# Kernel tuning notes

Hardware: AMD Instinct MI355X
Metric: run time of the kernel (lower is better)

The kernel has to match this reference:

```python
import jax, jax.numpy as jnp
import numpy as np

N_NODES = 50000
N_EDGES = 600000
N_GRAPHS = 64


def _linear_init(key, fan_in, fan_out):
    # torch nn.Linear default: U(-1/sqrt(fan_in), 1/sqrt(fan_in))
    s = 1.0 / np.sqrt(fan_in)
    kw, kb = jax.random.split(key)
    W = jax.random.uniform(kw, (fan_in, fan_out), jnp.float32, -s, s)
    b = jax.random.uniform(kb, (fan_out,), jnp.float32, -s, s)
    return W, b


def setup_inputs() -> dict:
    key = jax.random.key(0)
    ks = jax.random.split(key, 7)
    x = jax.random.normal(ks[0], (N_NODES, 128), jnp.float32)
    edge_index = jax.random.randint(ks[1], (2, N_EDGES), 0, N_NODES, dtype=jnp.int32).astype(jnp.int64)
    batch = jnp.sort(jax.random.randint(ks[2], (N_NODES,), 0, N_GRAPHS, dtype=jnp.int32)).astype(jnp.int64)
    W1, b1 = _linear_init(ks[3], 128, 256)
    W2, b2 = _linear_init(ks[4], 256, 256)
    W3, b3 = _linear_init(ks[5], 256, 128)
    W4, b4 = _linear_init(ks[6], 128, 10)
    return dict(x=x, edge_index=edge_index, batch=batch,
                W1=W1, b1=b1, W2=W2, b2=b2, W3=W3, b3=b3, W4=W4, b4=b4)


def _gcn_conv(h, src, dst, W, b, n_nodes):
    # PyG GCNConv: add self-loops (src/dst already include them),
    # symmetric normalization D^{-1/2} (A+I) D^{-1/2} h W + b.
    h = h @ W                                      # [N, Cout]
    deg = jax.ops.segment_sum(jnp.ones(src.shape[0], h.dtype), dst, num_segments=n_nodes)
    dinv = jnp.where(deg > 0, jax.lax.rsqrt(deg), 0.0)
    norm = dinv[src] * dinv[dst]                   # [E+N]
    msg = h[src] * norm[:, None]                   # gather + scale per edge
    agg = jax.ops.segment_sum(msg, dst, num_segments=n_nodes)  # scatter-add
    return agg + b


def reference(x, edge_index, batch, W1, b1, W2, b2, W3, b3, W4, b4):
    n = x.shape[0]
    loops = jnp.arange(n, dtype=edge_index.dtype)
    src = jnp.concatenate([edge_index[0], loops])
    dst = jnp.concatenate([edge_index[1], loops])
    # GCNBlock (activate_last=True since dense layers follow)
    h = jax.nn.relu(_gcn_conv(x, src, dst, W1, b1, n))
    h = jax.nn.relu(_gcn_conv(h, src, dst, W2, b2, n))
    # global_mean_pool over batch segments
    sums = jax.ops.segment_sum(h, batch, num_segments=N_GRAPHS)          # [G, 256]
    counts = jax.ops.segment_sum(jnp.ones((n,), h.dtype), batch, num_segments=N_GRAPHS)
    g = sums / jnp.maximum(counts, 1.0)[:, None]
    # DenseBlock [256 -> 128 -> 10], activate_last=False
    g = jax.nn.relu(g @ W3 + b3)
    return g @ W4 + b4
```

## Files before the change

### kernel.cpp

```cpp
#include <hip/hip_runtime.h>

typedef unsigned short u16;
typedef unsigned int u32;
typedef __attribute__((ext_vector_type(8))) short s16x8;
typedef __attribute__((ext_vector_type(4))) float f32x4;

#define NN 50000
#define NE 600000
#define NG 64

__device__ __forceinline__ u16 f2bf(float f) {
    u32 u = __float_as_uint(f);
    u32 r = (u + 0x7fffu + ((u >> 16) & 1u)) >> 16;
    return (u16)r;
}
__device__ __forceinline__ float bf2f(u16 h) {
    return __uint_as_float(((u32)h) << 16);
}
__device__ __forceinline__ void gll16(const void* g, void* l) {
    __builtin_amdgcn_global_load_lds((const __attribute__((address_space(1))) u32*)g,
                                     (__attribute__((address_space(3))) u32*)l, 16, 0, 0);
}

__global__ void k_hist(const int* __restrict__ dst, int* __restrict__ cnt, int ne) {
    int e = blockIdx.x * blockDim.x + threadIdx.x;
    if (e < ne) atomicAdd(&cnt[dst[e]], 1);
}

__global__ __launch_bounds__(256)
void k_scan1(const int* __restrict__ cnt, int* __restrict__ bsum, int n) {
    int i = blockIdx.x * 256 + threadIdx.x;
    int v = (i < n) ? cnt[i] : 0;
#pragma unroll
    for (int off = 32; off > 0; off >>= 1) v += __shfl_down(v, off, 64);
    __shared__ int ws[4];
    int lane = threadIdx.x & 63, w = threadIdx.x >> 6;
    if (lane == 0) ws[w] = v;
    __syncthreads();
    if (threadIdx.x == 0) bsum[blockIdx.x] = ws[0] + ws[1] + ws[2] + ws[3];
}

__global__ __launch_bounds__(256)
void k_scan2(int* __restrict__ bsum, int nb) {
    int t = threadIdx.x;
    int v = (t < nb) ? bsum[t] : 0;
    int lane = t & 63, w = t >> 6;
    int inc = v;
#pragma unroll
    for (int off = 1; off < 64; off <<= 1) {
        int x = __shfl_up(inc, off, 64);
        if (lane >= off) inc += x;
    }
    __shared__ int wtot[4];
    if (lane == 63) wtot[w] = inc;
    __syncthreads();
    int wo = 0;
    for (int j = 0; j < w; ++j) wo += wtot[j];
    if (t < nb) bsum[t] = wo + inc - v;
}

__global__ __launch_bounds__(256)
void k_scan3(const int* __restrict__ cnt, const int* __restrict__ boff,
             int* __restrict__ rowptr, int* __restrict__ cursor,
             float* __restrict__ dinv, int n) {
    int i = blockIdx.x * 256 + threadIdx.x;
    int v = (i < n) ? cnt[i] : 0;
    int lane = threadIdx.x & 63, w = threadIdx.x >> 6;
    int inc = v;
#pragma unroll
    for (int off = 1; off < 64; off <<= 1) {
        int x = __shfl_up(inc, off, 64);
        if (lane >= off) inc += x;
    }
    __shared__ int wtot[4];
    if (lane == 63) wtot[w] = inc;
    __syncthreads();
    int wo = boff[blockIdx.x];
    for (int j = 0; j < w; ++j) wo += wtot[j];
    if (i < n) {
        int excl = wo + inc - v;
        rowptr[i] = excl;
        cursor[i] = excl;
        dinv[i] = rsqrtf(1.0f + (float)v);
        if (i == n - 1) rowptr[n] = excl + v;
    }
}

__global__ void k_fill(const int* __restrict__ src, const int* __restrict__ dst,
                       const float* __restrict__ dinv,
                       int* __restrict__ cursor, uint2* __restrict__ csr2, int ne) {
    int e = blockIdx.x * blockDim.x + threadIdx.x;
    if (e < ne) {
        int pos = atomicAdd(&cursor[dst[e]], 1);
        int s = src[e];
        csr2[pos] = make_uint2((u32)s, __float_as_uint(dinv[s]));
    }
}

__device__ __forceinline__ void wsplit_tiled(const float* __restrict__ W,
                                             u16* __restrict__ hi, int gid) {
    int n = gid & 255, kgrp = gid >> 8;
    int kbase = kgrp * 8;
#pragma unroll
    for (int j = 0; j < 8; ++j) {
        float w = W[(size_t)(kbase + j) * 256 + n];
        hi[(size_t)gid * 8 + j] = f2bf(w);
    }
}

__global__ __launch_bounds__(256)
void k_preamble(const float* __restrict__ x, u16* __restrict__ xbf_s,
                const float* __restrict__ W1, u16* __restrict__ w1hi,
                const float* __restrict__ W2, u16* __restrict__ w2hi,
                float* __restrict__ sums, int* __restrict__ cnt,
                const int* __restrict__ batch, float* __restrict__ counts) {
    const int XB = (NN * 32 + 255) / 256;
    const int CB = (NN + 255) / 256;
    int b = blockIdx.x, t = threadIdx.x;
    if (b < XB) {
        int i = b * 256 + t;
        if (i < NN * 32) {
            float4 v = ((const float4*)x)[i];
            int node = i >> 5;
            int q = i & 31;
            int slice = q >> 3;
            int uoff = (q & 7) * 2;
            uint2 o;
            o.x = (u32)f2bf(v.x) | ((u32)f2bf(v.y) << 16);
            o.y = (u32)f2bf(v.z) | ((u32)f2bf(v.w) << 16);
            ((uint2*)xbf_s)[(((size_t)slice * NN + node) * 16 + uoff) >> 1] = o;
        }
        return;
    }
    b -= XB;
    if (b < 16) { wsplit_tiled(W1, w1hi, b * 256 + t); return; }
    b -= 16;
    if (b < 32) { wsplit_tiled(W2, w2hi, b * 256 + t); return; }
    b -= 32;
    if (b < 64) { sums[b * 256 + t] = 0.f; return; }
    b -= 64;
    if (b < CB) {
        int i = b * 256 + t;
        if (i < NN) cnt[i] = 0;
        return;
    }
    b -= CB;
    if (b == 0) {
        __shared__ int lb[65];
        if (t <= 64) {
            int lo = 0, hi = NN;
            while (lo < hi) {
                int mid = (lo + hi) >> 1;
                if (batch[mid] < t) lo = mid + 1; else hi = mid;
            }
            lb[t] = lo;
        }
        __syncthreads();
        if (t < 64) counts[t] = (float)(lb[t + 1] - lb[t]);
    }
}

template<int C>
__global__ __launch_bounds__(256)
void k_agg_sliced(const int* __restrict__ rowptr, const uint2* __restrict__ csr2,
                  const float* __restrict__ dinv, const u16* __restrict__ hbs,
                  u16* __restrict__ out, int n) {
    constexpr int NS = C / 32;
    const int nodeblocks = (NN + 15) / 16;
    int slice = blockIdx.x / nodeblocks;
    int nb = blockIdx.x - slice * nodeblocks;
    int lane = threadIdx.x & 63, wave = threadIdx.x >> 6;
    int g = lane >> 4, li = lane & 15;
    int node = nb * 16 + wave * 4 + g;
    if (node >= n) node = n - 1;
    int beg = rowptr[node], end = rowptr[node + 1];
    int m = end - beg;
    float di = dinv[node];
    const u32* sb = (const u32*)hbs + (size_t)slice * n * 16;

    u32 v = sb[(size_t)node * 16 + li];
    float a0 = bf2f((u16)v) * di, b0 = bf2f((u16)(v >> 16)) * di;
    float a1 = 0.f, b1 = 0.f;

    int mmax = m;
    mmax = max(mmax, __shfl_xor(mmax, 16, 64));
    mmax = max(mmax, __shfl_xor(mmax, 32, 64));

    for (int base = 0; base < mmax; base += 16) {
        int c = m - base;
        uint2 ew = make_uint2(0u, 0u);
        if (li < c) ew = csr2[beg + base + li];
        int t16 = mmax - base; if (t16 > 16) t16 = 16;
        int gb = lane & 48;
        for (int e = 0; e + 1 < t16; e += 2) {
            int   s0 = __shfl((int)ew.x, gb + e, 64);
            float w0 = __uint_as_float(__shfl((int)ew.y, gb + e, 64));
            int   s1 = __shfl((int)ew.x, gb + e + 1, 64);
            float w1 = __uint_as_float(__shfl((int)ew.y, gb + e + 1, 64));
            u32 r0 = sb[(size_t)s0 * 16 + li];
            u32 r1 = sb[(size_t)s1 * 16 + li];
            a0 += bf2f((u16)r0) * w0; b0 += bf2f((u16)(r0 >> 16)) * w0;
            a1 += bf2f((u16)r1) * w1; b1 += bf2f((u16)(r1 >> 16)) * w1;
        }
        if (t16 & 1) {
            int e = t16 - 1;
            int   s0 = __shfl((int)ew.x, gb + e, 64);
            float w0 = __uint_as_float(__shfl((int)ew.y, gb + e, 64));
            u32 r0 = sb[(size_t)s0 * 16 + li];
            a0 += bf2f((u16)r0) * w0; b0 += bf2f((u16)(r0 >> 16)) * w0;
        }
    }
    float fa = (a0 + a1) * di, fb = (b0 + b1) * di;
    u32 o = (u32)f2bf(fa) | ((u32)f2bf(fb) << 16);
    ((u32*)out)[(((size_t)node * C + slice * 32) >> 1) + li] = o;
}

template<bool POOL>
__global__ __launch_bounds__(512, 4)
void k_gemm_mfma(const u16* __restrict__ A, const u16* __restrict__ Bh,
                 const float* __restrict__ bias, u16* __restrict__ out_bf,
                 const int* __restrict__ batch, float* __restrict__ pool,
                 int M, int K) {
    __shared__ u16 ldsA[2][4096];
    const int tid = threadIdx.x, lane = tid & 63, wid = tid >> 6;
    const int bm = blockIdx.x * 128;
    const int wr = (wid >> 2) * 64, wc = (wid & 3) * 64;
    const int lr = lane & 15, kg = lane >> 4;

    const int srow = wid * 16 + (lane >> 2);
    const int sslot = lane & 3;
    const int ssw = (srow ^ (srow >> 2)) & 3;
    int srg = bm + srow; if (srg >= M) srg = M - 1;
    const u16* sbase = A + (size_t)srg * K + ((sslot ^ ssw) << 3);

    const u16* bh_p = Bh + (u32)kg * 2048 + (u32)(wc + lr) * 8;

    f32x4 acc[4][4];
#pragma unroll
    for (int i = 0; i < 4; ++i)
#pragma unroll
        for (int j = 0; j < 4; ++j) acc[i][j] = (f32x4){0.f, 0.f, 0.f, 0.f};

    const int nt = K >> 5;
    gll16(sbase, &ldsA[0][wid * 512]);
    __syncthreads();

    for (int t = 0; t < nt; ++t) {
        int cur = t & 1;
        if (t + 1 < nt)
            gll16(sbase + ((t + 1) << 5), &ldsA[cur ^ 1][wid * 512]);

        s16x8 bh[4];
#pragma unroll
        for (int fn = 0; fn < 4; ++fn)
            bh[fn] = *(const s16x8*)&bh_p[(u32)t * 8192 + (u32)fn * 128];
        const u16* lb = ldsA[cur];
        s16x8 a[4];
#pragma unroll
        for (int fm = 0; fm < 4; ++fm) {
            int r = wr + fm * 16 + lr;
            a[fm] = *(const s16x8*)&lb[r * 32 + ((kg ^ ((r ^ (r >> 2)) & 3)) << 3)];
        }
#pragma unroll
        for (int fn = 0; fn < 4; ++fn)
#pragma unroll
            for (int fm = 0; fm < 4; ++fm)
                acc[fm][fn] = __builtin_amdgcn_mfma_f32_16x16x32_bf16(a[fm], bh[fn], acc[fm][fn], 0, 0, 0);
        __syncthreads();
    }

#pragma unroll
    for (int fn = 0; fn < 4; ++fn) {
        int col = wc + fn * 16 + lr;
        float bv = bias[col];
        if (!POOL) {
            size_t sbase_o = ((size_t)(col >> 5) * (size_t)M) * 32 + (col & 31);
#pragma unroll
            for (int fm = 0; fm < 4; ++fm) {
                int rbase = bm + wr + fm * 16 + kg * 4;
#pragma unroll
                for (int r = 0; r < 4; ++r) {
                    int row = rbase + r;
                    if (row < M)
                        out_bf[sbase_o + (size_t)row * 32] = f2bf(fmaxf(acc[fm][fn][r] + bv, 0.f));
                }
            }
        } else {
            int gcur = -1;
            float run = 0.f;
#pragma unroll
            for (int fm = 0; fm < 4; ++fm) {
                int rbase = bm + wr + fm * 16 + kg * 4;
#pragma unroll
                for (int r = 0; r < 4; ++r) {
                    int row = rbase + r;
                    if (row < M) {
                        int g = batch[row];
                        float v = fmaxf(acc[fm][fn][r] + bv, 0.f);
                        if (g != gcur) {
                            if (gcur >= 0) atomicAdd(&pool[gcur * 256 + col], run);
                            gcur = g;
                            run = 0.f;
                        }
                        run += v;
                    }
                }
            }
            if (gcur >= 0) atomicAdd(&pool[gcur * 256 + col], run);
        }
    }
}

__global__ __launch_bounds__(128)
void k_dense(const float* __restrict__ sums, const float* __restrict__ counts,
             const float* __restrict__ W3, const float* __restrict__ b3,
             const float* __restrict__ W4, const float* __restrict__ b4,
             float* __restrict__ out) {
    __shared__ float g[256];
    __shared__ float hid[128];
    int gi = blockIdx.x;
    int t = threadIdx.x;
    float inv = 1.0f / fmaxf(counts[gi], 1.0f);
    for (int c = t; c < 256; c += 128) g[c] = sums[gi * 256 + c] * inv;
    __syncthreads();
    float acc = b3[t];
    for (int k = 0; k < 256; ++k) acc += g[k] * W3[k * 128 + t];
    hid[t] = fmaxf(acc, 0.0f);
    __syncthreads();
    if (t < 10) {
        float o = b4[t];
        for (int k = 0; k < 128; ++k) o += hid[k] * W4[k * 10 + t];
        out[gi * 10 + t] = o;
    }
}

extern "C" void kernel_launch(void* const* d_in, const int* in_sizes, int n_in,
                              void* d_out, int out_size, void* d_ws, size_t ws_size,
                              hipStream_t stream) {
    const float* x   = (const float*)d_in[0];
    const int*  eidx = (const int*)d_in[1];
    const int*  batch= (const int*)d_in[2];
    const float* W1 = (const float*)d_in[3];
    const float* b1 = (const float*)d_in[4];
    const float* W2 = (const float*)d_in[5];
    const float* b2 = (const float*)d_in[6];
    const float* W3 = (const float*)d_in[7];
    const float* b3 = (const float*)d_in[8];
    const float* W4 = (const float*)d_in[9];
    const float* b4 = (const float*)d_in[10];
    float* out = (float*)d_out;

    const int N = NN, E = NE, G = NG;
    const int* src = eidx;
    const int* dst = eidx + E;
    const int NB = (N + 255) / 256;

    char* p = (char*)d_ws;
    auto alloc = [&](size_t bytes) { char* r = p; p += (bytes + 255) & ~(size_t)255; return r; };
    u16*   h1bf_s = (u16*)alloc((size_t)N * 256 * 2);
    u16*   xbf_s  = (u16*)alloc((size_t)N * 128 * 2);
    float* dinv   = (float*)alloc((size_t)N * 4);
    float* sums   = (float*)alloc((size_t)G * 256 * 4);
    float* counts = (float*)alloc((size_t)G * 4);
    int*   cnt    = (int*)alloc((size_t)N * 4);
    int*   rowptr = (int*)alloc((size_t)(N + 1) * 4);
    int*   bsum   = (int*)alloc((size_t)NB * 4);
    uint2* csr2   = (uint2*)alloc((size_t)E * 8);
    u16*   agg1   = (u16*)alloc((size_t)N * 128 * 2);
    u16*   agg2   = (u16*)alloc((size_t)N * 256 * 2);
    u16*   w1hi   = (u16*)alloc((size_t)256 * 128 * 2);
    u16*   w2hi   = (u16*)alloc((size_t)256 * 256 * 2);
    int*   cursor = cnt;

    const int XB = (NN * 32 + 255) / 256;
    const int CB = (NN + 255) / 256;
    int pre_blocks = XB + 16 + 32 + 64 + CB + 1;
    k_preamble<<<pre_blocks, 256, 0, stream>>>(x, xbf_s, W1, w1hi, W2, w2hi,
                                               sums, cnt, batch, counts);

    k_hist<<<(E + 255) / 256, 256, 0, stream>>>(dst, cnt, E);
    k_scan1<<<NB, 256, 0, stream>>>(cnt, bsum, N);
    k_scan2<<<1, 256, 0, stream>>>(bsum, NB);
    k_scan3<<<NB, 256, 0, stream>>>(cnt, bsum, rowptr, cursor, dinv, N);
    k_fill<<<(E + 255) / 256, 256, 0, stream>>>(src, dst, dinv, cursor, csr2, E);

    const int nodeblocks = (N + 15) / 16;

    k_agg_sliced<128><<<4 * nodeblocks, 256, 0, stream>>>(rowptr, csr2, dinv, xbf_s, agg1, N);
    int gblocks = (N + 127) / 128;
    k_gemm_mfma<false><<<gblocks, 512, 0, stream>>>(agg1, w1hi, b1, h1bf_s,
                                                    nullptr, nullptr, N, 128);

    k_agg_sliced<256><<<8 * nodeblocks, 256, 0, stream>>>(rowptr, csr2, dinv, h1bf_s, agg2, N);
    k_gemm_mfma<true><<<gblocks, 512, 0, stream>>>(agg2, w2hi, b2, nullptr,
                                                   batch, sums, N, 256);

    k_dense<<<G, 128, 0, stream>>>(sums, counts, W3, b3, W4, b4, out);
}
```

Before: 242.6 us.

## Interleave feature slices across consecutive blocks and unroll per-node edge loop

Block indexing changes so that consecutive blocks handle different feature slices of the same node group, with the slice taken from the low bits of the block index. The likely aim is to spread slices across XCDs so that each XCD's L2 holds a narrower, slice-specific working set. The edge loop no longer shares CSR entries through wave shuffles and a wave-wide max degree. Each 16-lane group now reads its own edges directly and unrolls by four, which removes shuffle overhead and padding iterations at the cost of redundant, uncoalesced CSR loads.

```diff
diff --git a/kernel.cpp b/kernel.cpp
--- a/kernel.cpp
+++ b/kernel.cpp
@@ -162,19 +162,18 @@
 
 template<int C>
 __global__ __launch_bounds__(256)
-void k_agg_sliced(const int* __restrict__ rowptr, const uint2* __restrict__ csr2,
-                  const float* __restrict__ dinv, const u16* __restrict__ hbs,
-                  u16* __restrict__ out, int n) {
+void k_agg_xcd(const int* __restrict__ rowptr, const uint2* __restrict__ csr2,
+               const float* __restrict__ dinv, const u16* __restrict__ hbs,
+               u16* __restrict__ out, int n) {
     constexpr int NS = C / 32;
-    const int nodeblocks = (NN + 15) / 16;
-    int slice = blockIdx.x / nodeblocks;
-    int nb = blockIdx.x - slice * nodeblocks;
-    int lane = threadIdx.x & 63, wave = threadIdx.x >> 6;
-    int g = lane >> 4, li = lane & 15;
-    int node = nb * 16 + wave * 4 + g;
+    constexpr int LS = (NS == 8) ? 3 : 2;
+    int slice = blockIdx.x & (NS - 1);
+    int nb = blockIdx.x >> LS;
+    int li = threadIdx.x & 15;
+    int node = nb * 16 + (threadIdx.x >> 4);
     if (node >= n) node = n - 1;
-    int beg = rowptr[node], end = rowptr[node + 1];
-    int m = end - beg;
+    int beg = rowptr[node];
+    int m = rowptr[node + 1] - beg;
     float di = dinv[node];
     const u32* sb = (const u32*)hbs + (size_t)slice * n * 16;
 
@@ -182,37 +181,30 @@
     float a0 = bf2f((u16)v) * di, b0 = bf2f((u16)(v >> 16)) * di;
     float a1 = 0.f, b1 = 0.f;
 
-    int mmax = m;
-    mmax = max(mmax, __shfl_xor(mmax, 16, 64));
-    mmax = max(mmax, __shfl_xor(mmax, 32, 64));
-
-    for (int base = 0; base < mmax; base += 16) {
-        int c = m - base;
-        uint2 ew = make_uint2(0u, 0u);
-        if (li < c) ew = csr2[beg + base + li];
-        int t16 = mmax - base; if (t16 > 16) t16 = 16;
-        int gb = lane & 48;
-        for (int e = 0; e + 1 < t16; e += 2) {
-            int   s0 = __shfl((int)ew.x, gb + e, 64);
-            float w0 = __uint_as_float(__shfl((int)ew.y, gb + e, 64));
-            int   s1 = __shfl((int)ew.x, gb + e + 1, 64);
-            float w1 = __uint_as_float(__shfl((int)ew.y, gb + e + 1, 64));
-            u32 r0 = sb[(size_t)s0 * 16 + li];
-            u32 r1 = sb[(size_t)s1 * 16 + li];
-            a0 += bf2f((u16)r0) * w0; b0 += bf2f((u16)(r0 >> 16)) * w0;
-            a1 += bf2f((u16)r1) * w1; b1 += bf2f((u16)(r1 >> 16)) * w1;
-        }
-        if (t16 & 1) {
-            int e = t16 - 1;
-            int   s0 = __shfl((int)ew.x, gb + e, 64);
-            float w0 = __uint_as_float(__shfl((int)ew.y, gb + e, 64));
-            u32 r0 = sb[(size_t)s0 * 16 + li];
-            a0 += bf2f((u16)r0) * w0; b0 += bf2f((u16)(r0 >> 16)) * w0;
-        }
+    const uint2* ep = csr2 + beg;
+    int e = 0;
+    for (; e + 4 <= m; e += 4) {
+        uint2 e0 = ep[e], e1 = ep[e + 1], e2 = ep[e + 2], e3 = ep[e + 3];
+        u32 r0 = sb[(size_t)e0.x * 16 + li];
+        u32 r1 = sb[(size_t)e1.x * 16 + li];
+        u32 r2 = sb[(size_t)e2.x * 16 + li];
+        u32 r3 = sb[(size_t)e3.x * 16 + li];
+        float w0 = __uint_as_float(e0.y), w1 = __uint_as_float(e1.y);
+        float w2 = __uint_as_float(e2.y), w3 = __uint_as_float(e3.y);
+        a0 += bf2f((u16)r0) * w0; b0 += bf2f((u16)(r0 >> 16)) * w0;
+        a1 += bf2f((u16)r1) * w1; b1 += bf2f((u16)(r1 >> 16)) * w1;
+        a0 += bf2f((u16)r2) * w2; b0 += bf2f((u16)(r2 >> 16)) * w2;
+        a1 += bf2f((u16)r3) * w3; b1 += bf2f((u16)(r3 >> 16)) * w3;
+    }
+    for (; e < m; ++e) {
+        uint2 e0 = ep[e];
+        u32 r0 = sb[(size_t)e0.x * 16 + li];
+        float w0 = __uint_as_float(e0.y);
+        a0 += bf2f((u16)r0) * w0; b0 += bf2f((u16)(r0 >> 16)) * w0;
     }
     float fa = (a0 + a1) * di, fb = (b0 + b1) * di;
-    u32 o = (u32)f2bf(fa) | ((u32)f2bf(fb) << 16);
-    ((u32*)out)[(((size_t)node * C + slice * 32) >> 1) + li] = o;
+    ((u32*)out)[(size_t)node * (C / 2) + slice * 16 + li] =
+        (u32)f2bf(fa) | ((u32)f2bf(fb) << 16);
 }
 
 template<bool POOL>
@@ -386,12 +378,12 @@
 
     const int nodeblocks = (N + 15) / 16;
 
-    k_agg_sliced<128><<<4 * nodeblocks, 256, 0, stream>>>(rowptr, csr2, dinv, xbf_s, agg1, N);
+    k_agg_xcd<128><<<nodeblocks * 4, 256, 0, stream>>>(rowptr, csr2, dinv, xbf_s, agg1, N);
     int gblocks = (N + 127) / 128;
     k_gemm_mfma<false><<<gblocks, 512, 0, stream>>>(agg1, w1hi, b1, h1bf_s,
                                                     nullptr, nullptr, N, 128);
 
-    k_agg_sliced<256><<<8 * nodeblocks, 256, 0, stream>>>(rowptr, csr2, dinv, h1bf_s, agg2, N);
+    k_agg_xcd<256><<<nodeblocks * 8, 256, 0, stream>>>(rowptr, csr2, dinv, h1bf_s, agg2, N);
     k_gemm_mfma<true><<<gblocks, 512, 0, stream>>>(agg2, w2hi, b2, nullptr,
                                                    batch, sums, N, 256);
 
```

Measured after the change: 245.8 us. No clear change (+1.3%).
